# Kernel tuning notes

Measured on AMD Instinct MI355X. Metric: run time of the kernel, lower is better.

The kernel has to match this reference:

```python
import jax, jax.numpy as jnp
from jax import lax
import numpy as np

N, T, HID, COMB, ATT, K, D = 128, 64, 512, 1024, 128, 20, 2
FMAP = 64  # CNN output channels; feature map is 14x14 -> 196 locations
ODIM = K + 2 * K * D + K + 1  # 121 mixture-density output params


def setup_inputs() -> dict:
    key = jax.random.key(0)
    keys = iter(jax.random.split(key, 64))

    def rn(shape, s=0.05):
        return jax.random.normal(next(keys), shape, jnp.float32) * s

    inp = dict(
        x=rn((N, T, D), 1.0),
        x_canv=jax.random.uniform(next(keys), (N, 1, 28, 28), dtype=jnp.float32),
        start=rn((N, D), 1.0),
        conv1_w=rn((16, 1, 3, 3), 0.3), conv1_b=rn((16,)),
        conv2_w=rn((32, 16, 3, 3), 0.1), conv2_b=rn((32,)),
        conv3_w=rn((64, 32, 3, 3), 0.1), conv3_b=rn((64,)),
        init_w=rn((2 * HID, FMAP + 16)), init_b=rn((2 * HID,)),
        Uw=rn((ATT, HID)), Ub=rn((ATT,)),
        Ww=rn((ATT, FMAP)), Wb=rn((ATT,)),
        vw=rn((1, ATT)), vb=rn((1,)),
        beta_w=rn((FMAP, HID)), beta_b=rn((FMAP,)),
        xemb_w=rn((16, D), 0.5), xemb_b=rn((16,)),
        semb_w=rn((16, D), 0.5), semb_b=rn((16,)),
        Wih=rn((4 * HID, FMAP + 16)), Whh=rn((4 * HID, HID)),
        bih=rn((4 * HID,)), bhh=rn((4 * HID,)),
        comb_w=rn((COMB, FMAP + HID + 32)), comb_b=rn((COMB,)),
        out_w=rn((ODIM, COMB)), out_b=rn((ODIM,)),
    )
    return inp


def _conv(x, w, b, stride):
    # torch Conv2d(kernel=3, padding=1) with NCHW / OIHW layout
    y = lax.conv_general_dilated(x, w, (stride, stride), ((1, 1), (1, 1)),
                                 dimension_numbers=('NCHW', 'OIHW', 'NCHW'))
    return y + b[None, :, None, None]


def reference(x, x_canv, start, conv1_w, conv1_b, conv2_w, conv2_b, conv3_w, conv3_b,
              init_w, init_b, Uw, Ub, Ww, Wb, vw, vb, beta_w, beta_b,
              xemb_w, xemb_b, semb_w, semb_b, Wih, Whh, bih, bhh,
              comb_w, comb_b, out_w, out_b):
    n, Tt, d = x.shape
    # sequence_pad: prepend zero vector, drop last step
    xp = jnp.concatenate([jnp.zeros((n, 1, d), x.dtype), x[:, :-1]], axis=1)
    xe = jnp.tanh(xp @ xemb_w.T + xemb_b)          # (n,T,16)
    se = jnp.tanh(start @ semb_w.T + semb_b)       # (n,16)
    # CNN (zscore_canvases with new_stats=True)
    c = (x_canv - 0.0243) / 0.1383
    c = jax.nn.relu(_conv(c, conv1_w, conv1_b, 1))
    c = jax.nn.relu(_conv(c, conv2_w, conv2_b, 1))
    c = jnp.tanh(_conv(c, conv3_w, conv3_b, 2))    # (n,64,14,14)
    a = c.transpose(0, 2, 3, 1).reshape(n, -1, FMAP)  # (n,196,64)
    # Initialize LSTM state (num_layers=1)
    hidden = jnp.tanh(jnp.concatenate([a.mean(axis=1), se], axis=1) @ init_w.T + init_b)
    hidden = hidden.reshape(n, HID, 2)
    h0, c0 = hidden[:, :, 0], hidden[:, :, 1]
    # AttendSAT.register_annotation: precompute W(a)
    W_a = a @ Ww.T + Wb                             # (n,196,att)
    # dropout masks are keep-probs (eval / dropout=0) -> all ones, identity

    def step(carry, xt):
        h, cs = carry
        Uh = h @ Uw.T + Ub                          # (n,att)
        e = (jnp.tanh(W_a + Uh[:, None, :]) @ vw.T).squeeze(-1) + vb[0]
        alpha = jax.nn.softmax(e, axis=-1)          # (n,196)
        z = jnp.einsum('nlf,nl->nf', a, alpha)      # (n,64)
        z = jax.nn.sigmoid(h @ beta_w.T + beta_b) * z
        gates = jnp.concatenate([xt, z], axis=1) @ Wih.T + bih + h @ Whh.T + bhh
        gi, gf, gg, go = jnp.split(gates, 4, axis=1)  # torch gate order i,f,g,o
        cs = jax.nn.sigmoid(gf) * cs + jax.nn.sigmoid(gi) * jnp.tanh(gg)
        h = jax.nn.sigmoid(go) * jnp.tanh(cs)
        y = jnp.tanh(jnp.concatenate([h, z, xt, se], axis=1) @ comb_w.T + comb_b)
        y = y @ out_w.T + out_b
        return (h, cs), y

    _, ys = lax.scan(step, (h0, c0), xe.transpose(1, 0, 2))
    y_out = ys.transpose(1, 0, 2)                   # (n,T,121)
    # unpack_output
    mix, means, scales, corrs, vlog = jnp.split(
        y_out, [K, K + K * D, K + 2 * K * D, 2 * K + 2 * K * D], axis=-1)
    mix = jax.nn.softmax(mix, axis=-1)
    means = means.reshape(n, Tt, K, D)
    scales = jnp.exp(scales).reshape(n, Tt, K, D)
    corrs = jnp.tanh(corrs)
    return (mix, means, scales, corrs, vlog.squeeze(-1))
```

## Files before the change

kernel.cpp:

```cpp
#include <hip/hip_runtime.h>


#define TN 128
#define TT 64

typedef __attribute__((ext_vector_type(4))) float f32x4;
typedef __attribute__((ext_vector_type(8))) short bf16x8;

__device__ __forceinline__ float fsigm(float x){ return __builtin_amdgcn_rcpf(1.0f + __expf(-x)); }
__device__ __forceinline__ float ftanh(float x){ return 1.0f - 2.0f*__builtin_amdgcn_rcpf(1.0f + __expf(2.0f*x)); }
__device__ __forceinline__ unsigned short f2bf(float f){
  unsigned int u = __float_as_uint(f);
  u += 0x7fffu + ((u >> 16) & 1u);
  return (unsigned short)(u >> 16);
}
__device__ __forceinline__ float b2f(unsigned short u){ return __uint_as_float(((unsigned)u)<<16); }
__device__ __forceinline__ void cvt8(unsigned short* d, const float* s){
  __align__(16) unsigned short vals[8];
  #pragma unroll
  for (int j=0;j<8;j++) vals[j] = f2bf(s[j]);
  *(float4*)d = *(float4*)vals;
}

__device__ __forceinline__ void dev_conv1(int idx, const float* __restrict__ xc,
    const float* __restrict__ w, const float* __restrict__ b, unsigned short* __restrict__ c1bf){
  if (idx >= TN*16*784) return;
  int p = idx % 784, oc = (idx/784) & 15, n = idx/(784*16);
  int py = p/28, px = p%28;
  const float* src = xc + n*784;
  float acc = b[oc];
  #pragma unroll
  for (int ky=0;ky<3;ky++){
    int iy = py+ky-1; if (iy<0||iy>=28) continue;
    #pragma unroll
    for (int kx=0;kx<3;kx++){
      int ix = px+kx-1; if (ix<0||ix>=28) continue;
      acc += (src[iy*28+ix]-0.0243f)*(1.0f/0.1383f) * w[oc*9+ky*3+kx];
    }
  }
  c1bf[idx] = f2bf(fmaxf(acc, 0.0f));
}

__device__ __forceinline__ void dev_prep(int u,
    const float* __restrict__ Whh, const float* __restrict__ Wih,
    const float* __restrict__ bih, const float* __restrict__ bhh,
    const float* __restrict__ comb_w, const float* __restrict__ out_w, const float* __restrict__ out_b,
    const float* __restrict__ Uw, const float* __restrict__ beta_w, const float* __restrict__ Ww,
    const float* __restrict__ conv2_w, const float* __restrict__ conv3_w,
    unsigned short* __restrict__ wgf, float* __restrict__ gbias,
    unsigned short* __restrict__ cwbf, unsigned short* __restrict__ owbf, float* __restrict__ obias,
    unsigned short* __restrict__ uwbf, unsigned short* __restrict__ betabf, unsigned short* __restrict__ wwbf,
    unsigned short* __restrict__ w2b, unsigned short* __restrict__ w3b){
  if (u < 155648){
    int fragi = u >> 6, lane = u & 63;
    int g = fragi / 608, rem = fragi - g*608;
    int b = rem / 19, kt = rem - b*19;
    int row = g*512 + b*16 + (lane & 15);
    int col = kt*32 + (lane >> 4)*8;
    __align__(16) unsigned short vals[8];
    if (col < 512){
      const float* s = Whh + (size_t)row*512 + col;
      #pragma unroll
      for (int j=0;j<8;j++) vals[j] = f2bf(s[j]);
    } else if (col - 512 < 80){
      const float* s = Wih + (size_t)row*80 + (col-512);
      #pragma unroll
      for (int j=0;j<8;j++) vals[j] = f2bf(s[j]);
    } else {
      #pragma unroll
      for (int j=0;j<8;j++) vals[j] = 0;
    }
    *(float4*)(wgf + (size_t)u*8) = *(float4*)vals;
    return;
  }
  u -= 155648;
  if (u < 256){
    #pragma unroll
    for (int j=0;j<8;j++) gbias[u*8+j] = bih[u*8+j] + bhh[u*8+j];
    return;
  }
  u -= 256;
  if (u < 77824){ cvt8(cwbf + (size_t)u*8, comb_w + (size_t)u*8); return; }
  u -= 77824;
  if (u < 16384){
    int o = u >> 7, k2 = (u & 127)*8;
    __align__(16) unsigned short vals[8];
    if (o < 121){
      const float* s = out_w + (size_t)o*1024 + k2;
      #pragma unroll
      for (int j=0;j<8;j++) vals[j] = f2bf(s[j]);
    } else {
      #pragma unroll
      for (int j=0;j<8;j++) vals[j] = 0;
    }
    *(float4*)(owbf + (size_t)u*8) = *(float4*)vals;
    return;
  }
  u -= 16384;
  if (u < 16){
    #pragma unroll
    for (int j=0;j<8;j++){ int i = u*8+j; obias[i] = (i<121)? out_b[i] : 0.0f; }
    return;
  }
  u -= 16;
  if (u < 8192){ cvt8(uwbf + (size_t)u*8, Uw + (size_t)u*8); return; }
  u -= 8192;
  if (u < 4096){ cvt8(betabf + (size_t)u*8, beta_w + (size_t)u*8); return; }
  u -= 4096;
  if (u < 1024){ cvt8(wwbf + (size_t)u*8, Ww + (size_t)u*8); return; }
  u -= 1024;
  if (u < 640){
    int o = u/20, k2 = (u - o*20)*8;
    if (k2 < 144) cvt8(w2b + (size_t)u*8, conv2_w + (size_t)o*144 + k2);
    else { __align__(16) unsigned short z[8] = {0,0,0,0,0,0,0,0}; *(float4*)(w2b + (size_t)u*8) = *(float4*)z; }
    return;
  }
  u -= 640;
  if (u < 2560){
    int o = u/40, k2 = (u - o*40)*8;
    if (k2 < 288) cvt8(w3b + (size_t)u*8, conv3_w + (size_t)o*288 + k2);
    else { __align__(16) unsigned short z[8] = {0,0,0,0,0,0,0,0}; *(float4*)(w3b + (size_t)u*8) = *(float4*)z; }
    return;
  }
}

__global__ __launch_bounds__(256) void k_head(const float* __restrict__ xc,
    const float* __restrict__ conv1_w, const float* __restrict__ conv1_b, unsigned short* __restrict__ c1bf,
    const float* __restrict__ Whh, const float* __restrict__ Wih,
    const float* __restrict__ bih, const float* __restrict__ bhh,
    const float* __restrict__ comb_w, const float* __restrict__ out_w, const float* __restrict__ out_b,
    const float* __restrict__ Uw, const float* __restrict__ beta_w, const float* __restrict__ Ww,
    const float* __restrict__ conv2_w, const float* __restrict__ conv3_w,
    unsigned short* __restrict__ wgf, float* __restrict__ gbias,
    unsigned short* __restrict__ cwbf, unsigned short* __restrict__ owbf, float* __restrict__ obias,
    unsigned short* __restrict__ uwbf, unsigned short* __restrict__ betabf, unsigned short* __restrict__ wwbf,
    unsigned short* __restrict__ w2b, unsigned short* __restrict__ w3b){
  int bid = blockIdx.x;
  if (bid < 6272) dev_conv1(bid*256 + threadIdx.x, xc, conv1_w, conv1_b, c1bf);
  else dev_prep((bid-6272)*256 + threadIdx.x, Whh, Wih, bih, bhh, comb_w, out_w, out_b,
                Uw, beta_w, Ww, conv2_w, conv3_w,
                wgf, gbias, cwbf, owbf, obias, uwbf, betabf, wwbf, w2b, w3b);
}

__global__ __launch_bounds__(256) void k_im2col2(const unsigned short* __restrict__ c1bf, unsigned short* __restrict__ a2){
  int u = blockIdx.x*256 + threadIdx.x;
  if (u >= 100352*20) return;
  int r = u / 20, k8 = (u - r*20)*8;
  int p = r % 784, n = r / 784;
  int py = p/28, px = p%28;
  __align__(16) unsigned short vals[8];
  #pragma unroll
  for (int j=0;j<8;j++){
    int k = k8 + j;
    unsigned short v = 0;
    if (k < 144){
      int ic = k/9, rem = k - ic*9, ky = rem/3, kx = rem - ky*3;
      int iy = py+ky-1, ix = px+kx-1;
      if (iy>=0 && iy<28 && ix>=0 && ix<28) v = c1bf[(n*16+ic)*784 + iy*28+ix];
    }
    vals[j] = v;
  }
  *(float4*)(a2 + (size_t)r*160 + k8) = *(float4*)vals;
}

__global__ __launch_bounds__(256) void k_gconv2(const unsigned short* __restrict__ a2,
    const unsigned short* __restrict__ w2b, const float* __restrict__ b2,
    unsigned short* __restrict__ c2bf){
  int mbase = blockIdx.x*128;
  int tid = threadIdx.x, w = tid>>6, l = tid&63;
  int lr = l&15, lk = (l>>4)*8;
  __shared__ unsigned short at[128*168];
  {
    int row = tid>>1, off = (tid&1)*80;
    const unsigned short* sp = a2 + (size_t)(mbase+row)*160 + off;
    #pragma unroll
    for (int j=0;j<10;j++) *(float4*)&at[row*168 + off + j*8] = *(const float4*)(sp + j*8);
  }
  __syncthreads();
  f32x4 acc[2][2];
  #pragma unroll
  for (int mi=0;mi<2;mi++){ acc[mi][0]=(f32x4){0,0,0,0}; acc[mi][1]=(f32x4){0,0,0,0}; }
  for (int kt=0; kt<5; ++kt){
    bf16x8 b0 = *(const bf16x8*)(w2b + (0*16+lr)*160 + kt*32 + lk);
    bf16x8 b1 = *(const bf16x8*)(w2b + (1*16+lr)*160 + kt*32 + lk);
    #pragma unroll
    for (int mi=0;mi<2;mi++){
      bf16x8 afrag = *(const bf16x8*)&at[((2*w+mi)*16+lr)*168 + kt*32 + lk];
      acc[mi][0] = __builtin_amdgcn_mfma_f32_16x16x32_bf16(afrag, b0, acc[mi][0], 0,0,0);
      acc[mi][1] = __builtin_amdgcn_mfma_f32_16x16x32_bf16(afrag, b1, acc[mi][1], 0,0,0);
    }
  }
  #pragma unroll
  for (int mi=0;mi<2;mi++){
    #pragma unroll
    for (int j=0;j<2;j++){
      int oc = j*16 + lr;
      float bb = b2[oc];
      #pragma unroll
      for (int i=0;i<4;i++){
        int r = mbase + (2*w+mi)*16 + (l>>4)*4 + i;
        c2bf[(size_t)r*32 + oc] = f2bf(fmaxf(acc[mi][j][i] + bb, 0.0f));
      }
    }
  }
}

__global__ __launch_bounds__(256) void k_im2col3(const unsigned short* __restrict__ c2bf, unsigned short* __restrict__ a3){
  int u = blockIdx.x*256 + threadIdx.x;
  if (u >= 25088*40) return;
  int r = u / 40, k8 = (u - r*40)*8;
  int p = r % 196, n = r / 196;
  int py = p/14, px = p%14;
  __align__(16) unsigned short vals[8];
  #pragma unroll
  for (int j=0;j<8;j++){
    int k = k8 + j;
    unsigned short v = 0;
    if (k < 288){
      int ic = k/9, rem = k - ic*9, ky = rem/3, kx = rem - ky*3;
      int iy = 2*py+ky-1, ix = 2*px+kx-1;
      if (iy>=0 && iy<28 && ix>=0 && ix<28) v = c2bf[(size_t)(n*784 + iy*28+ix)*32 + ic];
    }
    vals[j] = v;
  }
  *(float4*)(a3 + (size_t)r*320 + k8) = *(float4*)vals;
}

__global__ __launch_bounds__(256) void k_gconv3(const unsigned short* __restrict__ a3,
    const unsigned short* __restrict__ w3b, const float* __restrict__ b3,
    unsigned short* __restrict__ afbf, unsigned short* __restrict__ abf){
  int mbase = blockIdx.x*128;
  int tid = threadIdx.x, w = tid>>6, l = tid&63;
  int lr = l&15, lk = (l>>4)*8;
  __shared__ unsigned short at[128*168];
  f32x4 acc[2][4];
  #pragma unroll
  for (int mi=0;mi<2;mi++)
    #pragma unroll
    for (int j=0;j<4;j++) acc[mi][j]=(f32x4){0,0,0,0};
  for (int kt2=0; kt2<2; ++kt2){
    {
      int row = tid>>1, off = (tid&1)*80;
      const unsigned short* sp = a3 + (size_t)(mbase+row)*320 + kt2*160 + off;
      #pragma unroll
      for (int j=0;j<10;j++) *(float4*)&at[row*168 + off + j*8] = *(const float4*)(sp + j*8);
    }
    __syncthreads();
    for (int kt=0; kt<5; ++kt){
      #pragma unroll
      for (int mi=0;mi<2;mi++){
        bf16x8 afrag = *(const bf16x8*)&at[((2*w+mi)*16+lr)*168 + kt*32 + lk];
        #pragma unroll
        for (int j=0;j<4;j++){
          bf16x8 bf = *(const bf16x8*)(w3b + (size_t)(j*16+lr)*320 + kt2*160 + kt*32 + lk);
          acc[mi][j] = __builtin_amdgcn_mfma_f32_16x16x32_bf16(afrag, bf, acc[mi][j], 0,0,0);
        }
      }
    }
    __syncthreads();
  }
  #pragma unroll
  for (int mi=0;mi<2;mi++){
    #pragma unroll
    for (int j=0;j<4;j++){
      int oc = j*16 + lr;
      float bb = b3[oc];
      #pragma unroll
      for (int i=0;i<4;i++){
        int r = mbase + (2*w+mi)*16 + (l>>4)*4 + i;
        int n = r/196, p = r - n*196;
        float v = ftanh(acc[mi][j][i] + bb);
        unsigned short vb16 = f2bf(v);
        afbf[(size_t)(n*64+oc)*196 + p] = vb16;
        abf[(size_t)r*64 + oc] = vb16;
      }
    }
  }
}

__global__ __launch_bounds__(256) void k_mid(
    const unsigned short* __restrict__ afbf,
    const float* __restrict__ start, const float* __restrict__ sw, const float* __restrict__ sb,
    const unsigned short* __restrict__ abf, const unsigned short* __restrict__ wwbf,
    const float* __restrict__ Wb, unsigned short* __restrict__ wabf,
    const float* __restrict__ x, const float* __restrict__ xw, const float* __restrict__ xb,
    unsigned short* __restrict__ cbf, unsigned short* __restrict__ ubf_all,
    const float* __restrict__ init_w, const float* __restrict__ init_b,
    unsigned short* __restrict__ hbfA, float* __restrict__ cbuf)
{
  const int bid = blockIdx.x, tid = threadIdx.x;
  __shared__ __align__(16) unsigned short at[128*40];
  __shared__ float qp[4][64];
  __shared__ float am[64];
  __shared__ float sse[16];
  if (bid < 196){
    int mbase = bid*128;
    int w = tid>>6, l = tid&63;
    int lr = l & 15, lk = (l>>4)*8;
    f32x4 acc[8][2];
    #pragma unroll
    for (int m=0;m<8;m++){ acc[m][0] = (f32x4){0,0,0,0}; acc[m][1] = (f32x4){0,0,0,0}; }
    for (int kt=0; kt<2; ++kt){
      int row = tid>>1, half = (tid&1)*16;
      const unsigned short* sp = abf + (mbase+row)*64 + kt*32 + half;
      *(float4*)&at[row*40 + half]     = *(const float4*)sp;
      *(float4*)&at[row*40 + half + 8] = *(const float4*)(sp + 8);
      __syncthreads();
      bf16x8 b0 = *(const bf16x8*)(wwbf + ((2*w+0)*16 + lr)*64 + kt*32 + lk);
      bf16x8 b1 = *(const bf16x8*)(wwbf + ((2*w+1)*16 + lr)*64 + kt*32 + lk);
      #pragma unroll
      for (int m=0;m<8;m++){
        bf16x8 afrag = *(const bf16x8*)&at[(m*16+lr)*40 + lk];
        acc[m][0] = __builtin_amdgcn_mfma_f32_16x16x32_bf16(afrag, b0, acc[m][0], 0,0,0);
        acc[m][1] = __builtin_amdgcn_mfma_f32_16x16x32_bf16(afrag, b1, acc[m][1], 0,0,0);
      }
      __syncthreads();
    }
    #pragma unroll
    for (int m=0;m<8;m++){
      #pragma unroll
      for (int j=0;j<2;j++){
        int att = (2*w+j)*16 + lr;
        float wb = Wb[att];
        #pragma unroll
        for (int i=0;i<4;i++){
          int arow = mbase + m*16 + (l>>4)*4 + i;
          int n = arow/196, l2 = arow - n*196;
          wabf[((size_t)n*196 + l2)*128 + att] = f2bf(acc[m][j][i] + wb);
        }
      }
    }
    return;
  }
  if (bid < 2244){
    int idx = (bid-196)*256 + tid;
    if (idx >= TN*TT*64) return;
    int j = idx & 63, r = idx >> 6;
    int n = r >> 6, t = r & 63;
    if (j < 16){
      float acc = xb[j];
      if (t > 0){ const float* xp = x + (n*TT + t-1)*2; acc += xp[0]*xw[j*2] + xp[1]*xw[j*2+1]; }
      cbf[(size_t)r*608 + 576 + j] = f2bf(ftanh(acc));
    } else if (j < 32){
      int jj = j-16;
      cbf[(size_t)r*608 + 592 + jj] = f2bf(ftanh(sb[jj] + start[n*2]*sw[jj*2] + start[n*2+1]*sw[jj*2+1]));
    } else if (j < 48){
      int jj = j-32;
      float acc = xb[jj];
      if (t > 0){ const float* xp = x + (n*TT + t-1)*2; acc += xp[0]*xw[jj*2] + xp[1]*xw[jj*2+1]; }
      ubf_all[((size_t)t*TN + n)*96 + jj] = f2bf(ftanh(acc));
    } else {
      ubf_all[((size_t)t*TN + n)*96 + 80 + (j-48)] = 0;
    }
    return;
  }
  {
    const int n = bid - 2244;
    int f = tid & 63, q = tid >> 6;
    const unsigned short* row = afbf + (size_t)(n*64+f)*196 + q*49;
    float s = 0;
    #pragma unroll 7
    for (int l=0;l<49;l++) s += b2f(row[l]);
    qp[q][f] = s;
    __syncthreads();
    if (tid < 64) am[tid] = (qp[0][tid]+qp[1][tid]+qp[2][tid]+qp[3][tid]) * (1.0f/196.0f);
    else if (tid < 80){
      int j = tid-64;
      sse[j] = ftanh(sb[j] + start[n*2]*sw[j*2] + start[n*2+1]*sw[j*2+1]);
    }
    __syncthreads();
    #pragma unroll
    for (int k=0;k<4;k++){
      int o = tid + k*256;
      const float* wr = init_w + (size_t)o*80;
      float acc = init_b[o];
      #pragma unroll 8
      for (int k2=0;k2<64;k2++) acc += am[k2]*wr[k2];
      #pragma unroll
      for (int k2=0;k2<16;k2++) acc += sse[k2]*wr[64+k2];
      float v = ftanh(acc);
      if (o & 1) cbuf[n*512 + (o>>1)] = v;
      else       hbfA[n*512 + (o>>1)] = f2bf(v);
    }
  }
}

__global__ __launch_bounds__(512) void k_stepA(int t,
    const unsigned short* __restrict__ hbf_in,
    const unsigned short* __restrict__ uwbf, const float* __restrict__ Ub,
    const unsigned short* __restrict__ betabf, const float* __restrict__ beta_b,
    const float* __restrict__ vw, const float* __restrict__ vb,
    const unsigned short* __restrict__ wabf, const unsigned short* __restrict__ afbf,
    unsigned short* __restrict__ ubf_all, unsigned short* __restrict__ cbf,
    const unsigned short* __restrict__ wgf, float* __restrict__ gpart)
{
  const int bid = blockIdx.x, tid = threadIdx.x;
  __shared__ __align__(16) float hs[512];
  __shared__ __align__(16) float Uh[128];
  __shared__ __align__(16) float vws[128];
  __shared__ float bsig[64];
  __shared__ float ew[196];
  __shared__ float red[8];
  __shared__ float up[4][128];
  __shared__ float qp8[8][64];
  __shared__ float ep2[256][2];
  __shared__ __align__(16) unsigned short at2[128*516];

  if (bid < TN){
    const int n = bid;
    hs[tid] = b2f(hbf_in[n*512 + tid]);
    if (tid < 128) vws[tid] = vw[tid];
    const float vb0 = vb[0];
    __syncthreads();
    {
      int att = tid & 127, q = tid >> 7;
      const unsigned short* uw = uwbf + (size_t)att*512 + q*128;
      const float* hh = hs + q*128;
      float acc = 0.f;
      #pragma unroll 4
      for (int k=0;k<128;k+=8){
        bf16x8 v = *(const bf16x8*)(uw + k);
        acc += hh[k+0]*b2f(v[0]) + hh[k+1]*b2f(v[1]) + hh[k+2]*b2f(v[2]) + hh[k+3]*b2f(v[3])
             + hh[k+4]*b2f(v[4]) + hh[k+5]*b2f(v[5]) + hh[k+6]*b2f(v[6]) + hh[k+7]*b2f(v[7]);
      }
      up[q][att] = acc;
    }
    {
      int f = tid & 63, q = tid >> 6;
      const unsigned short* bw = betabf + (size_t)f*512 + q*64;
      const float* hh = hs + q*64;
      float acc = 0.f;
      #pragma unroll 4
      for (int k=0;k<64;k+=8){
        bf16x8 v = *(const bf16x8*)(bw + k);
        acc += hh[k+0]*b2f(v[0]) + hh[k+1]*b2f(v[1]) + hh[k+2]*b2f(v[2]) + hh[k+3]*b2f(v[3])
             + hh[k+4]*b2f(v[4]) + hh[k+5]*b2f(v[5]) + hh[k+6]*b2f(v[6]) + hh[k+7]*b2f(v[7]);
      }
      qp8[q][f] = acc;
    }
    __syncthreads();
    if (tid < 128) Uh[tid] = Ub[tid] + up[0][tid]+up[1][tid]+up[2][tid]+up[3][tid];
    else if (tid < 192){
      int f = tid-128;
      bsig[f] = fsigm(beta_b[f] + qp8[0][f]+qp8[1][f]+qp8[2][f]+qp8[3][f]
                                + qp8[4][f]+qp8[5][f]+qp8[6][f]+qp8[7][f]);
    }
    __syncthreads();
    {
      int l = tid >> 1, half = tid & 1;
      float acc = 0.f;
      if (l < 196){
        const unsigned short* wr = wabf + ((size_t)n*196 + l)*128 + half*64;
        const float* uh = Uh + half*64;
        const float* vv = vws + half*64;
        #pragma unroll 2
        for (int k=0;k<64;k+=8){
          bf16x8 wv = *(const bf16x8*)(wr + k);
          acc += vv[k+0]*ftanh(b2f(wv[0]) + uh[k+0]) + vv[k+1]*ftanh(b2f(wv[1]) + uh[k+1])
               + vv[k+2]*ftanh(b2f(wv[2]) + uh[k+2]) + vv[k+3]*ftanh(b2f(wv[3]) + uh[k+3])
               + vv[k+4]*ftanh(b2f(wv[4]) + uh[k+4]) + vv[k+5]*ftanh(b2f(wv[5]) + uh[k+5])
               + vv[k+6]*ftanh(b2f(wv[6]) + uh[k+6]) + vv[k+7]*ftanh(b2f(wv[7]) + uh[k+7]);
        }
      }
      ep2[l][half] = acc;
    }
    __syncthreads();
    float ex = 0.f;
    if (tid < 196) ex = __expf(vb0 + ep2[tid][0] + ep2[tid][1]);
    float ss = ex;
    #pragma unroll
    for (int off=32; off>0; off>>=1) ss += __shfl_xor(ss, off);
    if ((tid&63)==0) red[tid>>6] = ss;
    if (tid<196) ew[tid] = ex;
    __syncthreads();
    float inv = __builtin_amdgcn_rcpf(red[0]+red[1]+red[2]+red[3]+red[4]+red[5]+red[6]+red[7]);
    {
      int f = tid & 63, q = tid >> 6;
      int l0 = q*25, l1 = (l0+25 < 196) ? l0+25 : 196;
      const unsigned short* an = afbf + (size_t)n*12544 + (size_t)f*196;
      float acc = 0.f;
      for (int l2=l0; l2<l1; l2++) acc += ew[l2]*b2f(an[l2]);
      qp8[q][f] = acc;
    }
    __syncthreads();
    if (tid < 64){
      float z = bsig[tid]*(qp8[0][tid]+qp8[1][tid]+qp8[2][tid]+qp8[3][tid]
                          +qp8[4][tid]+qp8[5][tid]+qp8[6][tid]+qp8[7][tid])*inv;
      unsigned short zb = f2bf(z);
      ubf_all[((size_t)t*TN + n)*96 + 16 + tid] = zb;
      cbf[((size_t)n*TT + t)*608 + 512 + tid] = zb;
    }
  } else {
    const int b = bid - TN;
    const int w = tid>>6, l = tid&63, lr = l&15, li = l>>4, lk = li*8;
    const int g = w & 3, mh = w >> 2;
    bf16x8 wreg[16];
    {
      const unsigned short* wp = wgf + ((size_t)(g*32 + b)*19)*512 + (size_t)l*8;
      #pragma unroll
      for (int i=0;i<16;i++) wreg[i] = *(const bf16x8*)(wp + (size_t)i*512);
    }
    for (int i = tid; i < 8192; i += 512){
      int row = i >> 6, seg = (i & 63)*8;
      *(float4*)&at2[row*516 + seg] = *(const float4*)(hbf_in + (size_t)row*512 + seg);
    }
    __syncthreads();
    f32x4 acc[4];
    #pragma unroll
    for (int m2=0;m2<4;m2++) acc[m2] = (f32x4){0,0,0,0};
    #pragma unroll 4
    for (int kt=0; kt<16; ++kt){
      #pragma unroll
      for (int m2=0;m2<4;m2++){
        bf16x8 a = *(const bf16x8*)&at2[((mh*4+m2)*16 + lr)*516 + kt*32 + lk];
        acc[m2] = __builtin_amdgcn_mfma_f32_16x16x32_bf16(a, wreg[kt], acc[m2], 0,0,0);
      }
    }
    #pragma unroll
    for (int m2=0;m2<4;m2++){
      #pragma unroll
      for (int i=0;i<4;i++){
        int n2 = (mh*4+m2)*16 + li*4 + i;
        gpart[(((size_t)(g*32 + b)*128 + n2)<<4) + lr] = acc[m2][i];
      }
    }
  }
}

__global__ __launch_bounds__(512) void k_stepB(int t,
    unsigned short* __restrict__ hout,
    const unsigned short* __restrict__ ubf_all,
    const unsigned short* __restrict__ wgf, const float* __restrict__ gbias,
    const float* __restrict__ gpart,
    float* __restrict__ cbuf, unsigned short* __restrict__ cbf)
{
  const int b = blockIdx.x, tid = threadIdx.x;
  const int w = tid>>6, l = tid&63, lr = l&15, li = l>>4, lk = li*8;
  const int g = w & 3, mh = w >> 2;
  __shared__ float gsh[4][128][16];
  const unsigned short* ub = ubf_all + (size_t)t*TN*96;
  bf16x8 wz[3];
  {
    const unsigned short* wp = wgf + (((size_t)(g*32 + b)*19) + 16)*512 + (size_t)l*8;
    #pragma unroll
    for (int i=0;i<3;i++) wz[i] = *(const bf16x8*)(wp + (size_t)i*512);
  }
  for (int i = tid; i < 2048; i += 512){
    int gg = i>>9, r = i&511;
    *(float4*)&gsh[gg][r>>2][(r&3)*4] = *(const float4*)&gpart[(((size_t)(gg*32 + b)*128)<<4) + r*4];
  }
  f32x4 acc[4];
  #pragma unroll
  for (int m2=0;m2<4;m2++) acc[m2] = (f32x4){0,0,0,0};
  #pragma unroll
  for (int kt=0; kt<3; ++kt){
    #pragma unroll
    for (int m2=0;m2<4;m2++){
      bf16x8 a = *(const bf16x8*)(ub + (size_t)((mh*4+m2)*16 + lr)*96 + kt*32 + lk);
      acc[m2] = __builtin_amdgcn_mfma_f32_16x16x32_bf16(a, wz[kt], acc[m2], 0,0,0);
    }
  }
  __syncthreads();
  #pragma unroll
  for (int m2=0;m2<4;m2++)
    #pragma unroll
    for (int i=0;i<4;i++)
      gsh[g][(mh*4+m2)*16 + li*4 + i][lr] += acc[m2][i];
  __syncthreads();
  #pragma unroll
  for (int e=0;e<4;++e){
    int c = tid*4 + e;
    int nn = c>>4, j = c&15;
    int hidx = b*16 + j;
    float gi = gsh[0][nn][j] + gbias[         hidx];
    float gf = gsh[1][nn][j] + gbias[1*512 + hidx];
    float gg = gsh[2][nn][j] + gbias[2*512 + hidx];
    float go = gsh[3][nn][j] + gbias[3*512 + hidx];
    float cc = cbuf[nn*512 + hidx];
    float cs = fsigm(gf)*cc + fsigm(gi)*ftanh(gg);
    float h  = fsigm(go)*ftanh(cs);
    cbuf[nn*512 + hidx] = cs;
    unsigned short hb = f2bf(h);
    hout[nn*512 + hidx] = hb;
    cbf[((size_t)nn*TT + t)*608 + hidx] = hb;
  }
}

__global__ __launch_bounds__(256) void k_comb(const unsigned short* __restrict__ cbf,
    const unsigned short* __restrict__ cwbf, const float* __restrict__ comb_b,
    unsigned short* __restrict__ ybf){
  int mbase = blockIdx.x*128, obase = blockIdx.y*128;
  int tid = threadIdx.x, w = tid>>6, l = tid&63;
  int lr = l&15, lk = (l>>4)*8;
  __shared__ unsigned short at[128*40];
  f32x4 acc[8][2];
  #pragma unroll
  for (int m=0;m<8;m++){ acc[m][0] = (f32x4){0,0,0,0}; acc[m][1] = (f32x4){0,0,0,0}; }
  for (int kt=0; kt<19; ++kt){
    int row = tid>>1, half = (tid&1)*16;
    const unsigned short* sp = cbf + (size_t)(mbase+row)*608 + kt*32 + half;
    *(float4*)&at[row*40 + half]     = *(const float4*)sp;
    *(float4*)&at[row*40 + half + 8] = *(const float4*)(sp + 8);
    __syncthreads();
    bf16x8 b0 = *(const bf16x8*)(cwbf + (size_t)(obase + (2*w+0)*16 + lr)*608 + kt*32 + lk);
    bf16x8 b1 = *(const bf16x8*)(cwbf + (size_t)(obase + (2*w+1)*16 + lr)*608 + kt*32 + lk);
    #pragma unroll
    for (int m=0;m<8;m++){
      bf16x8 afrag = *(const bf16x8*)&at[(m*16+lr)*40 + lk];
      acc[m][0] = __builtin_amdgcn_mfma_f32_16x16x32_bf16(afrag, b0, acc[m][0], 0,0,0);
      acc[m][1] = __builtin_amdgcn_mfma_f32_16x16x32_bf16(afrag, b1, acc[m][1], 0,0,0);
    }
    __syncthreads();
  }
  #pragma unroll
  for (int m=0;m<8;m++){
    #pragma unroll
    for (int j=0;j<2;j++){
      int o = obase + (2*w+j)*16 + lr;
      float cb = comb_b[o];
      #pragma unroll
      for (int i=0;i<4;i++){
        int r = mbase + m*16 + (l>>4)*4 + i;
        ybf[(size_t)r*1024 + o] = f2bf(ftanh(acc[m][j][i] + cb));
      }
    }
  }
}

__global__ __launch_bounds__(256) void k_out(const unsigned short* __restrict__ ybf,
    const unsigned short* __restrict__ owbf, const float* __restrict__ obias,
    float* __restrict__ out){
  int mbase = blockIdx.x*128;
  int tid = threadIdx.x, w = tid>>6, l = tid&63;
  int lr = l&15, lk = (l>>4)*8;
  __shared__ unsigned short at[128*40];
  __shared__ float osh[128][129];
  f32x4 acc[8][2];
  #pragma unroll
  for (int m=0;m<8;m++){ acc[m][0] = (f32x4){0,0,0,0}; acc[m][1] = (f32x4){0,0,0,0}; }
  for (int kt=0; kt<32; ++kt){
    int row = tid>>1, half = (tid&1)*16;
    const unsigned short* sp = ybf + (size_t)(mbase+row)*1024 + kt*32 + half;
    *(float4*)&at[row*40 + half]     = *(const float4*)sp;
    *(float4*)&at[row*40 + half + 8] = *(const float4*)(sp + 8);
    __syncthreads();
    bf16x8 b0 = *(const bf16x8*)(owbf + ((2*w+0)*16 + lr)*1024 + kt*32 + lk);
    bf16x8 b1 = *(const bf16x8*)(owbf + ((2*w+1)*16 + lr)*1024 + kt*32 + lk);
    #pragma unroll
    for (int m=0;m<8;m++){
      bf16x8 afrag = *(const bf16x8*)&at[(m*16+lr)*40 + lk];
      acc[m][0] = __builtin_amdgcn_mfma_f32_16x16x32_bf16(afrag, b0, acc[m][0], 0,0,0);
      acc[m][1] = __builtin_amdgcn_mfma_f32_16x16x32_bf16(afrag, b1, acc[m][1], 0,0,0);
    }
    __syncthreads();
  }
  #pragma unroll
  for (int m=0;m<8;m++){
    #pragma unroll
    for (int j=0;j<2;j++){
      int o = (2*w+j)*16 + lr;
      float ob = obias[o];
      #pragma unroll
      for (int i=0;i<4;i++){
        int r = m*16 + (l>>4)*4 + i;
        osh[r][o] = acc[m][j][i] + ob;
      }
    }
  }
  __syncthreads();
  if (tid < 128){
    const float* row = osh[tid];
    int r = mbase + tid;
    float mx = -1e30f;
    #pragma unroll
    for (int k2=0;k2<20;k2++) mx = fmaxf(mx, row[k2]);
    float e[20]; float s = 0;
    #pragma unroll
    for (int k2=0;k2<20;k2++){ e[k2] = __expf(row[k2]-mx); s += e[k2]; }
    float inv = __builtin_amdgcn_rcpf(s);
    float* mixo  = out;
    float* meano = out + 163840;
    float* scaleo= out + 491520;
    float* corro = out + 819200;
    float* vlogo = out + 983040;
    #pragma unroll
    for (int k2=0;k2<20;k2++) mixo[r*20+k2] = e[k2]*inv;
    #pragma unroll
    for (int j=0;j<40;j++) meano[r*40+j] = row[20+j];
    #pragma unroll
    for (int j=0;j<40;j++) scaleo[r*40+j] = __expf(row[60+j]);
    #pragma unroll
    for (int k2=0;k2<20;k2++) corro[r*20+k2] = ftanh(row[100+k2]);
    vlogo[r] = row[120];
  }
}

extern "C" void kernel_launch(void* const* d_in, const int* in_sizes, int n_in,
                              void* d_out, int out_size, void* d_ws, size_t ws_size,
                              hipStream_t stream){
  const float* x       = (const float*)d_in[0];
  const float* x_canv  = (const float*)d_in[1];
  const float* start_  = (const float*)d_in[2];
  const float* conv1_w = (const float*)d_in[3];
  const float* conv1_b = (const float*)d_in[4];
  const float* conv2_w = (const float*)d_in[5];
  const float* conv2_b = (const float*)d_in[6];
  const float* conv3_w = (const float*)d_in[7];
  const float* conv3_b = (const float*)d_in[8];
  const float* init_w  = (const float*)d_in[9];
  const float* init_b  = (const float*)d_in[10];
  const float* Uw      = (const float*)d_in[11];
  const float* Ub      = (const float*)d_in[12];
  const float* Ww      = (const float*)d_in[13];
  const float* Wb      = (const float*)d_in[14];
  const float* vw      = (const float*)d_in[15];
  const float* vb      = (const float*)d_in[16];
  const float* beta_w  = (const float*)d_in[17];
  const float* beta_b  = (const float*)d_in[18];
  const float* xemb_w  = (const float*)d_in[19];
  const float* xemb_b  = (const float*)d_in[20];
  const float* semb_w  = (const float*)d_in[21];
  const float* semb_b  = (const float*)d_in[22];
  const float* Wih     = (const float*)d_in[23];
  const float* Whh     = (const float*)d_in[24];
  const float* bih     = (const float*)d_in[25];
  const float* bhh     = (const float*)d_in[26];
  const float* comb_w  = (const float*)d_in[27];
  const float* comb_b  = (const float*)d_in[28];
  const float* out_w   = (const float*)d_in[29];
  const float* out_b   = (const float*)d_in[30];
  (void)in_sizes; (void)n_in; (void)out_size; (void)ws_size;

  char* wsb = (char*)d_ws;
  size_t off = 0;
  auto alloc = [&](size_t bytes)->char*{
    char* p = wsb + off;
    off = (off + bytes + 255) & ~(size_t)255;
    return p;
  };
  unsigned short* c1bf   = (unsigned short*)alloc((size_t)TN*16*784*2);
  unsigned short* a2     = (unsigned short*)alloc((size_t)100352*160*2);
  unsigned short* a3     = a2;
  unsigned short* c2bf   = (unsigned short*)alloc((size_t)100352*32*2);
  unsigned short* afbf   = (unsigned short*)alloc((size_t)TN*64*196*2);
  unsigned short* abf    = (unsigned short*)alloc((size_t)TN*196*64*2);
  unsigned short* wabf   = (unsigned short*)alloc((size_t)TN*196*128*2);
  float*          cbuf   = (float*)alloc((size_t)TN*512*4);
  unsigned short* hbfA   = (unsigned short*)alloc((size_t)TN*512*2);
  unsigned short* hbfB   = (unsigned short*)alloc((size_t)TN*512*2);
  unsigned short* ubf_all= (unsigned short*)alloc((size_t)TT*TN*96*2);
  unsigned short* cbf    = (unsigned short*)alloc((size_t)TN*TT*608*2);
  unsigned short* ybf    = (unsigned short*)alloc((size_t)TN*TT*1024*2);
  unsigned short* wgf    = (unsigned short*)alloc((size_t)1245184*2);
  float*          gbias  = (float*)alloc((size_t)2048*4);
  float*          gpart  = (float*)alloc((size_t)4*128*512*4);
  unsigned short* cwbf   = (unsigned short*)alloc((size_t)1024*608*2);
  unsigned short* owbf   = (unsigned short*)alloc((size_t)128*1024*2);
  float*          obias  = (float*)alloc((size_t)128*4);
  unsigned short* uwbf   = (unsigned short*)alloc((size_t)128*512*2);
  unsigned short* betabf = (unsigned short*)alloc((size_t)64*512*2);
  unsigned short* wwbf   = (unsigned short*)alloc((size_t)128*64*2);
  unsigned short* w2b    = (unsigned short*)alloc((size_t)32*160*2);
  unsigned short* w3b    = (unsigned short*)alloc((size_t)64*320*2);

  hipLaunchKernelGGL(k_head, dim3(7314), dim3(256), 0, stream,
                     x_canv, conv1_w, conv1_b, c1bf,
                     Whh, Wih, bih, bhh, comb_w, out_w, out_b, Uw, beta_w, Ww, conv2_w, conv3_w,
                     wgf, gbias, cwbf, owbf, obias, uwbf, betabf, wwbf, w2b, w3b);
  hipLaunchKernelGGL(k_im2col2, dim3(7840), dim3(256), 0, stream, c1bf, a2);
  hipLaunchKernelGGL(k_gconv2, dim3(784), dim3(256), 0, stream, a2, w2b, conv2_b, c2bf);
  hipLaunchKernelGGL(k_im2col3, dim3(3920), dim3(256), 0, stream, c2bf, a3);
  hipLaunchKernelGGL(k_gconv3, dim3(196), dim3(256), 0, stream, a3, w3b, conv3_b, afbf, abf);
  hipLaunchKernelGGL(k_mid, dim3(2372), dim3(256), 0, stream,
                     afbf, start_, semb_w, semb_b,
                     abf, wwbf, Wb, wabf,
                     x, xemb_w, xemb_b, cbf, ubf_all,
                     init_w, init_b, hbfA, cbuf);

  for (int t = 0; t < TT; ++t){
    unsigned short* hin  = (t & 1) ? hbfB : hbfA;
    unsigned short* hout = (t & 1) ? hbfA : hbfB;
    hipLaunchKernelGGL(k_stepA, dim3(160), dim3(512), 0, stream, t,
                       hin, uwbf, Ub, betabf, beta_b, vw, vb, wabf, afbf, ubf_all, cbf, wgf, gpart);
    hipLaunchKernelGGL(k_stepB, dim3(32), dim3(512), 0, stream, t,
                       hout, ubf_all, wgf, gbias, gpart, cbuf, cbf);
  }

  hipLaunchKernelGGL(k_comb, dim3(64, 8), dim3(256), 0, stream, cbf, cwbf, comb_b, ybf);
  hipLaunchKernelGGL(k_out, dim3(64), dim3(256), 0, stream, ybf, owbf, obias, (float*)d_out);
}
```

Baseline: 1.449 ms.

## Fuse LSTM step kernels into one launch with redundant cell recomputation

```diff
diff --git a/kernel.cpp b/kernel.cpp
--- a/kernel.cpp
+++ b/kernel.cpp
@@ -286,7 +286,7 @@
     const float* __restrict__ x, const float* __restrict__ xw, const float* __restrict__ xb,
     unsigned short* __restrict__ cbf, unsigned short* __restrict__ ubf_all,
     const float* __restrict__ init_w, const float* __restrict__ init_b,
-    unsigned short* __restrict__ hbfA, float* __restrict__ cbuf)
+    unsigned short* __restrict__ hbf0, float* __restrict__ cbufA)
 {
   const int bid = blockIdx.x, tid = threadIdx.x;
   __shared__ __align__(16) unsigned short at[128*40];
@@ -379,20 +379,22 @@
       #pragma unroll
       for (int k2=0;k2<16;k2++) acc += sse[k2]*wr[64+k2];
       float v = ftanh(acc);
-      if (o & 1) cbuf[n*512 + (o>>1)] = v;
-      else       hbfA[n*512 + (o>>1)] = f2bf(v);
-    }
-  }
-}
-
-__global__ __launch_bounds__(512) void k_stepA(int t,
-    const unsigned short* __restrict__ hbf_in,
+      if (o & 1) cbufA[n*512 + (o>>1)] = v;
+      else       hbf0[n*512 + (o>>1)] = f2bf(v);
+    }
+  }
+}
+
+__global__ __launch_bounds__(512) void k_step(int t,
+    const unsigned short* __restrict__ hbf0,
+    const float* __restrict__ cbuf_in, float* __restrict__ cbuf_out,
+    const unsigned short* __restrict__ gp_in, unsigned short* __restrict__ gp_out,
     const unsigned short* __restrict__ uwbf, const float* __restrict__ Ub,
     const unsigned short* __restrict__ betabf, const float* __restrict__ beta_b,
     const float* __restrict__ vw, const float* __restrict__ vb,
     const unsigned short* __restrict__ wabf, const unsigned short* __restrict__ afbf,
     unsigned short* __restrict__ ubf_all, unsigned short* __restrict__ cbf,
-    const unsigned short* __restrict__ wgf, float* __restrict__ gpart)
+    const unsigned short* __restrict__ wgf, const float* __restrict__ gbias)
 {
   const int bid = blockIdx.x, tid = threadIdx.x;
   __shared__ __align__(16) float hs[512];
@@ -404,14 +406,48 @@
   __shared__ float up[4][128];
   __shared__ float qp8[8][64];
   __shared__ float ep2[256][2];
+  __shared__ unsigned short ush[96];
   __shared__ __align__(16) unsigned short at2[128*516];
 
   if (bid < TN){
     const int n = bid;
-    hs[tid] = b2f(hbf_in[n*512 + tid]);
     if (tid < 128) vws[tid] = vw[tid];
     const float vb0 = vb[0];
-    __syncthreads();
+    if (t == 0){
+      hs[tid] = b2f(hbf0[n*512 + tid]);
+      __syncthreads();
+    } else {
+      if (tid < 96) ush[tid] = ubf_all[((size_t)(t-1)*TN + n)*96 + tid];
+      __syncthreads();
+      const int bb = tid>>4, lr2 = tid&15;
+      const int ntile = n>>4, rr = n&15;
+      float gate[4];
+      #pragma unroll
+      for (int g=0; g<4; ++g){
+        float acc = 0.f;
+        #pragma unroll
+        for (int kt=0; kt<3; ++kt){
+          const unsigned short* wp = wgf + (size_t)((g*32+bb)*19 + 16 + kt)*512;
+          #pragma unroll
+          for (int q=0; q<4; ++q){
+            bf16x8 wv = *(const bf16x8*)(wp + (lr2 + 16*q)*8);
+            const unsigned short* uu = ush + kt*32 + q*8;
+            #pragma unroll
+            for (int j=0;j<8;j++) acc += b2f(uu[j]) * b2f((unsigned short)wv[j]);
+          }
+        }
+        acc += b2f(gp_in[(size_t)((g*32+bb)*8 + ntile)*256 + ((rr>>2)*16 + lr2)*4 + (rr&3)]);
+        gate[g] = acc + gbias[g*512 + tid];
+      }
+      float c_old = cbuf_in[n*512 + tid];
+      float cs = fsigm(gate[1])*c_old + fsigm(gate[0])*ftanh(gate[2]);
+      float h  = fsigm(gate[3])*ftanh(cs);
+      cbuf_out[n*512 + tid] = cs;
+      hs[tid] = h;
+      cbf[((size_t)n*TT + (t-1))*608 + tid] = f2bf(h);
+      __syncthreads();
+    }
+    if (t == TT) return;
     {
       int att = tid & 127, q = tid >> 7;
       const unsigned short* uw = uwbf + (size_t)att*512 + q*128;
@@ -491,6 +527,7 @@
       cbf[((size_t)n*TT + t)*608 + 512 + tid] = zb;
     }
   } else {
+    if (t == TT) return;
     const int b = bid - TN;
     const int w = tid>>6, l = tid&63, lr = l&15, li = l>>4, lk = li*8;
     const int g = w & 3, mh = w >> 2;
@@ -500,11 +537,47 @@
       #pragma unroll
       for (int i=0;i<16;i++) wreg[i] = *(const bf16x8*)(wp + (size_t)i*512);
     }
-    for (int i = tid; i < 8192; i += 512){
-      int row = i >> 6, seg = (i & 63)*8;
-      *(float4*)&at2[row*516 + seg] = *(const float4*)(hbf_in + (size_t)row*512 + seg);
-    }
-    __syncthreads();
+    if (t == 0){
+      for (int i = tid; i < 8192; i += 512){
+        int row = i >> 6, seg = (i & 63)*8;
+        *(float4*)&at2[row*516 + seg] = *(const float4*)(hbf0 + (size_t)row*512 + seg);
+      }
+      __syncthreads();
+    } else {
+      const unsigned short* ub = ubf_all + (size_t)(t-1)*TN*96;
+      bf16x8 uf[3];
+      #pragma unroll
+      for (int kt=0;kt<3;kt++) uf[kt] = *(const bf16x8*)(ub + (size_t)(w*16 + lr)*96 + kt*32 + lk);
+      for (int hc=0; hc<32; ++hc){
+        f32x4 gg4[4];
+        #pragma unroll
+        for (int gg=0; gg<4; ++gg){
+          f32x4 acc = (f32x4){0,0,0,0};
+          #pragma unroll
+          for (int kt=0;kt<3;kt++){
+            bf16x8 wzf = *(const bf16x8*)(wgf + (size_t)((gg*32+hc)*19 + 16 + kt)*512 + (size_t)l*8);
+            acc = __builtin_amdgcn_mfma_f32_16x16x32_bf16(uf[kt], wzf, acc, 0,0,0);
+          }
+          ushort4 gp4 = *(const ushort4*)(gp_in + (size_t)((gg*32+hc)*8 + w)*256 + l*4);
+          float gb = gbias[gg*512 + hc*16 + lr];
+          acc[0] += b2f(gp4.x) + gb;
+          acc[1] += b2f(gp4.y) + gb;
+          acc[2] += b2f(gp4.z) + gb;
+          acc[3] += b2f(gp4.w) + gb;
+          gg4[gg] = acc;
+        }
+        #pragma unroll
+        for (int i=0;i<4;i++){
+          int smp = w*16 + li*4 + i;
+          int hcol = hc*16 + lr;
+          float c_old = cbuf_in[smp*512 + hcol];
+          float cs = fsigm(gg4[1][i])*c_old + fsigm(gg4[0][i])*ftanh(gg4[2][i]);
+          float h  = fsigm(gg4[3][i])*ftanh(cs);
+          at2[smp*516 + hcol] = f2bf(h);
+        }
+      }
+      __syncthreads();
+    }
     f32x4 acc[4];
     #pragma unroll
     for (int m2=0;m2<4;m2++) acc[m2] = (f32x4){0,0,0,0};
@@ -518,71 +591,11 @@
     }
     #pragma unroll
     for (int m2=0;m2<4;m2++){
-      #pragma unroll
-      for (int i=0;i<4;i++){
-        int n2 = (mh*4+m2)*16 + li*4 + i;
-        gpart[(((size_t)(g*32 + b)*128 + n2)<<4) + lr] = acc[m2][i];
-      }
-    }
-  }
-}
-
-__global__ __launch_bounds__(512) void k_stepB(int t,
-    unsigned short* __restrict__ hout,
-    const unsigned short* __restrict__ ubf_all,
-    const unsigned short* __restrict__ wgf, const float* __restrict__ gbias,
-    const float* __restrict__ gpart,
-    float* __restrict__ cbuf, unsigned short* __restrict__ cbf)
-{
-  const int b = blockIdx.x, tid = threadIdx.x;
-  const int w = tid>>6, l = tid&63, lr = l&15, li = l>>4, lk = li*8;
-  const int g = w & 3, mh = w >> 2;
-  __shared__ float gsh[4][128][16];
-  const unsigned short* ub = ubf_all + (size_t)t*TN*96;
-  bf16x8 wz[3];
-  {
-    const unsigned short* wp = wgf + (((size_t)(g*32 + b)*19) + 16)*512 + (size_t)l*8;
-    #pragma unroll
-    for (int i=0;i<3;i++) wz[i] = *(const bf16x8*)(wp + (size_t)i*512);
-  }
-  for (int i = tid; i < 2048; i += 512){
-    int gg = i>>9, r = i&511;
-    *(float4*)&gsh[gg][r>>2][(r&3)*4] = *(const float4*)&gpart[(((size_t)(gg*32 + b)*128)<<4) + r*4];
-  }
-  f32x4 acc[4];
-  #pragma unroll
-  for (int m2=0;m2<4;m2++) acc[m2] = (f32x4){0,0,0,0};
-  #pragma unroll
-  for (int kt=0; kt<3; ++kt){
-    #pragma unroll
-    for (int m2=0;m2<4;m2++){
-      bf16x8 a = *(const bf16x8*)(ub + (size_t)((mh*4+m2)*16 + lr)*96 + kt*32 + lk);
-      acc[m2] = __builtin_amdgcn_mfma_f32_16x16x32_bf16(a, wz[kt], acc[m2], 0,0,0);
-    }
-  }
-  __syncthreads();
-  #pragma unroll
-  for (int m2=0;m2<4;m2++)
-    #pragma unroll
-    for (int i=0;i<4;i++)
-      gsh[g][(mh*4+m2)*16 + li*4 + i][lr] += acc[m2][i];
-  __syncthreads();
-  #pragma unroll
-  for (int e=0;e<4;++e){
-    int c = tid*4 + e;
-    int nn = c>>4, j = c&15;
-    int hidx = b*16 + j;
-    float gi = gsh[0][nn][j] + gbias[         hidx];
-    float gf = gsh[1][nn][j] + gbias[1*512 + hidx];
-    float gg = gsh[2][nn][j] + gbias[2*512 + hidx];
-    float go = gsh[3][nn][j] + gbias[3*512 + hidx];
-    float cc = cbuf[nn*512 + hidx];
-    float cs = fsigm(gf)*cc + fsigm(gi)*ftanh(gg);
-    float h  = fsigm(go)*ftanh(cs);
-    cbuf[nn*512 + hidx] = cs;
-    unsigned short hb = f2bf(h);
-    hout[nn*512 + hidx] = hb;
-    cbf[((size_t)nn*TT + t)*608 + hidx] = hb;
+      ushort4 st;
+      st.x = f2bf(acc[m2][0]); st.y = f2bf(acc[m2][1]);
+      st.z = f2bf(acc[m2][2]); st.w = f2bf(acc[m2][3]);
+      *(ushort4*)(gp_out + (size_t)((g*32 + b)*8 + (mh*4+m2))*256 + l*4) = st;
+    }
   }
 }
 
@@ -745,15 +758,16 @@
   unsigned short* afbf   = (unsigned short*)alloc((size_t)TN*64*196*2);
   unsigned short* abf    = (unsigned short*)alloc((size_t)TN*196*64*2);
   unsigned short* wabf   = (unsigned short*)alloc((size_t)TN*196*128*2);
-  float*          cbuf   = (float*)alloc((size_t)TN*512*4);
-  unsigned short* hbfA   = (unsigned short*)alloc((size_t)TN*512*2);
-  unsigned short* hbfB   = (unsigned short*)alloc((size_t)TN*512*2);
+  float*          cbufA  = (float*)alloc((size_t)TN*512*4);
+  float*          cbufB  = (float*)alloc((size_t)TN*512*4);
+  unsigned short* hbf0   = (unsigned short*)alloc((size_t)TN*512*2);
   unsigned short* ubf_all= (unsigned short*)alloc((size_t)TT*TN*96*2);
   unsigned short* cbf    = (unsigned short*)alloc((size_t)TN*TT*608*2);
   unsigned short* ybf    = (unsigned short*)alloc((size_t)TN*TT*1024*2);
   unsigned short* wgf    = (unsigned short*)alloc((size_t)1245184*2);
   float*          gbias  = (float*)alloc((size_t)2048*4);
-  float*          gpart  = (float*)alloc((size_t)4*128*512*4);
+  unsigned short* gpA    = (unsigned short*)alloc((size_t)262144*2);
+  unsigned short* gpB    = (unsigned short*)alloc((size_t)262144*2);
   unsigned short* cwbf   = (unsigned short*)alloc((size_t)1024*608*2);
   unsigned short* owbf   = (unsigned short*)alloc((size_t)128*1024*2);
   float*          obias  = (float*)alloc((size_t)128*4);
@@ -775,15 +789,17 @@
                      afbf, start_, semb_w, semb_b,
                      abf, wwbf, Wb, wabf,
                      x, xemb_w, xemb_b, cbf, ubf_all,
-                     init_w, init_b, hbfA, cbuf);
-
-  for (int t = 0; t < TT; ++t){
-    unsigned short* hin  = (t & 1) ? hbfB : hbfA;
-    unsigned short* hout = (t & 1) ? hbfA : hbfB;
-    hipLaunchKernelGGL(k_stepA, dim3(160), dim3(512), 0, stream, t,
-                       hin, uwbf, Ub, betabf, beta_b, vw, vb, wabf, afbf, ubf_all, cbf, wgf, gpart);
-    hipLaunchKernelGGL(k_stepB, dim3(32), dim3(512), 0, stream, t,
-                       hout, ubf_all, wgf, gbias, gpart, cbuf, cbf);
+                     init_w, init_b, hbf0, cbufA);
+
+  for (int t = 0; t <= TT; ++t){
+    const unsigned short* gp_in = ((t+1)&1) ? gpB : gpA;
+    unsigned short*       gp_out = (t&1) ? gpB : gpA;
+    const float* c_in  = (t&1) ? cbufA : cbufB;
+    float*       c_out = (t&1) ? cbufB : cbufA;
+    hipLaunchKernelGGL(k_step, dim3(160), dim3(512), 0, stream, t,
+                       hbf0, c_in, c_out, gp_in, gp_out,
+                       uwbf, Ub, betabf, beta_b, vw, vb, wabf, afbf,
+                       ubf_all, cbf, wgf, gbias);
   }
 
   hipLaunchKernelGGL(k_comb, dim3(64, 8), dim3(256), 0, stream, cbf, cwbf, comb_b, ybf);
```

Measured after the change: 3.156 ms. 118% more time.
